# Kernel tuning notes

Measured on AMD Instinct MI355X. Metric: run time of the kernel, lower is better.

Reference implementation:

```python
import jax, jax.numpy as jnp
import numpy as np

EPS_OT = 0.1        # args.model.ot_reg
N_ITERS = 5         # args.model.ot_transport
COS_EPS = 1e-8      # torch F.cosine_similarity eps
L2_EPS = 1e-12      # torch F.normalize eps
LN_EPS = 1e-5       # nn.LayerNorm default eps
IN_DIM, HID = 768, 256


def setup_inputs() -> dict:
    key = jax.random.key(0)
    ks = jax.random.split(key, 8)
    Ba, Bb, Sa, Sb = 48, 48, 96, 96
    s_in = 1.0 / np.sqrt(IN_DIM)
    return {
        "batch_a": jax.random.normal(ks[0], (Ba, Sa, IN_DIM), jnp.float32),
        "batch_b": jax.random.normal(ks[1], (Bb, Sb, IN_DIM), jnp.float32),
        "Wq": jax.random.normal(ks[2], (IN_DIM, HID), jnp.float32) * s_in,
        "bq": jnp.zeros((HID,), jnp.float32),
        "Wk": jax.random.normal(ks[3], (IN_DIM, HID), jnp.float32) * s_in,
        "bk": jnp.zeros((HID,), jnp.float32),
        "Wv": jax.random.normal(ks[4], (IN_DIM, HID), jnp.float32) * s_in,
        "bv": jnp.zeros((HID,), jnp.float32),
        "ln_g": jnp.ones((HID,), jnp.float32),
        "ln_b": jnp.zeros((HID,), jnp.float32),
    }


def _layernorm(x, g, b):
    mu = jnp.mean(x, axis=-1, keepdims=True)
    var = jnp.var(x, axis=-1, keepdims=True)
    return (x - mu) * jax.lax.rsqrt(var + LN_EPS) * g + b


def _sinkhorn(C):
    # multiplicative Sinkhorn on kernel exp(C/eps); row/col renormalization
    T = jnp.exp(C / EPS_OT)  # [Ba,Bb,Sa,Sb]
    def body(_, T):
        T = T / jnp.sum(T, axis=-1, keepdims=True)
        T = T / jnp.sum(T, axis=-2, keepdims=True)
        return T
    return jax.lax.fori_loop(0, N_ITERS, body, T)


def reference(batch_a, batch_b, Wq, bq, Wk, bk, Wv, bv, ln_g, ln_b):
    q = batch_a @ Wq + bq          # [Ba,Sa,H]
    k = batch_b @ Wk + bk          # [Bb,Sb,H]
    v = batch_b @ Wv + bv          # [Bb,Sb,H]

    # cosine similarity across batches: [Ba,Bb,Sa,Sb]
    qn = q / jnp.maximum(jnp.linalg.norm(q, axis=-1, keepdims=True), COS_EPS)
    kn = k / jnp.maximum(jnp.linalg.norm(k, axis=-1, keepdims=True), COS_EPS)
    C = jnp.einsum('aid,bjd->abij', qn, kn)

    T = jax.lax.stop_gradient(_sinkhorn(C))  # C.detach() in source
    # F.normalize(dim=-1): L2 over last dim
    T = T / jnp.maximum(jnp.linalg.norm(T, axis=-1, keepdims=True), L2_EPS)
    # dropout p=0.0 -> identity (eval)

    attended = jnp.einsum('abij,bjd->abid', T, v) + q[:, None]  # [Ba,Bb,Sa,H]
    return _layernorm(attended, ln_g, ln_b)
```

## Files before the change

kernel.cpp:

```cpp
#include <hip/hip_runtime.h>
#include <hip/hip_bf16.h>

typedef __attribute__((ext_vector_type(4))) float f32x4;
typedef __attribute__((ext_vector_type(2))) float f32x2;
typedef __attribute__((ext_vector_type(8))) short bf16x8;
typedef __attribute__((ext_vector_type(4))) short s16x4;

#define BA 48
#define BB 48
#define SS 96
#define DIN 768
#define HH 256

static __device__ __forceinline__ short f2bf(float f) {
    __hip_bfloat16 h = __float2bfloat16(f);
    return *reinterpret_cast<short*>(&h);
}

static __device__ __forceinline__ f32x4 mfma16(bf16x8 a, bf16x8 b, f32x4 c) {
    return __builtin_amdgcn_mfma_f32_16x16x32_bf16(a, b, c, 0, 0, 0);
}

__global__ __launch_bounds__(256) void wt_kernel(
    const float* __restrict__ Wq, const float* __restrict__ Wk,
    const float* __restrict__ Wv, short* __restrict__ wt) {
    __shared__ float tile[64][65];
    int k0 = blockIdx.x * 64, n0 = blockIdx.y * 64, mat = blockIdx.z;
    const float* W = (mat == 0) ? Wq : (mat == 1) ? Wk : Wv;
    int t = threadIdx.x;
#pragma unroll
    for (int j = 0; j < 16; ++j) {
        int kk = j * 4 + (t >> 6);
        int nn = t & 63;
        tile[kk][nn] = W[(size_t)(k0 + kk) * HH + n0 + nn];
    }
    __syncthreads();
#pragma unroll
    for (int j = 0; j < 4; ++j) {
        int nn = j * 16 + (t >> 4);
        int kk = (t & 15) * 4;
        s16x4 pk;
#pragma unroll
        for (int i = 0; i < 4; ++i) pk[i] = f2bf(tile[kk + i][nn]);
        *reinterpret_cast<s16x4*>(&wt[(size_t)(mat * HH + n0 + nn) * DIN + k0 + kk]) = pk;
    }
}

__global__ __launch_bounds__(256) void xbf_kernel(
    const float* __restrict__ Xa, const float* __restrict__ Xb,
    short* __restrict__ xa, short* __restrict__ xb) {
    size_t i = (size_t)blockIdx.x * 256 + threadIdx.x;
    const float* src;
    short* dst;
    size_t off;
    if (i < 442368) { src = Xa; dst = xa; off = i * 8; }
    else            { src = Xb; dst = xb; off = (i - 442368) * 8; }
    f32x4 a = *reinterpret_cast<const f32x4*>(src + off);
    f32x4 b = *reinterpret_cast<const f32x4*>(src + off + 4);
    bf16x8 o;
    o[0] = f2bf(a[0]); o[1] = f2bf(a[1]); o[2] = f2bf(a[2]); o[3] = f2bf(a[3]);
    o[4] = f2bf(b[0]); o[5] = f2bf(b[1]); o[6] = f2bf(b[2]); o[7] = f2bf(b[3]);
    *reinterpret_cast<bf16x8*>(dst + off) = o;
}

__global__ __launch_bounds__(384) void qkv_kernel(
    const short* __restrict__ xa, const short* __restrict__ xb,
    const float* __restrict__ bq, const float* __restrict__ bk, const float* __restrict__ bv,
    const short* __restrict__ wt,
    float* __restrict__ q_ws, float* __restrict__ k_ws, short* __restrict__ vt_ws) {
    __shared__ short vtile[64][104];

    int bb = blockIdx.x;
    int mat = blockIdx.y;
    int c0 = blockIdx.z * 64;
    int tid = threadIdx.x;
    int wave = tid >> 6, lane = tid & 63;
    int c = lane & 15, g = lane >> 4;

    const short* X = ((mat == 0) ? xa : xb) + (size_t)bb * SS * DIN;
    const short* Wt = wt + (size_t)mat * HH * DIN;
    const float* bias = (mat == 0) ? bq : (mat == 1) ? bk : bv;

    const f32x4 z4 = {0.f, 0.f, 0.f, 0.f};
    f32x4 acc[4];
#pragma unroll
    for (int n = 0; n < 4; ++n) acc[n] = z4;

    const short* ap = X + (16 * wave + c) * DIN + g * 8;
    const short* bp = Wt + (c0 + c) * DIN + g * 8;
    for (int kk = 0; kk < DIN; kk += 32) {
        bf16x8 af = *reinterpret_cast<const bf16x8*>(ap + kk);
#pragma unroll
        for (int n = 0; n < 4; ++n) {
            bf16x8 bf = *reinterpret_cast<const bf16x8*>(bp + n * 16 * DIN + kk);
            acc[n] = mfma16(af, bf, acc[n]);
        }
    }
#pragma unroll
    for (int n = 0; n < 4; ++n) {
        float bv_ = bias[c0 + n * 16 + c];
#pragma unroll
        for (int r = 0; r < 4; ++r) acc[n][r] += bv_;
    }

    if (mat < 2) {
        float* dst = (mat == 0) ? q_ws : k_ws;
#pragma unroll
        for (int n = 0; n < 4; ++n)
#pragma unroll
            for (int r = 0; r < 4; ++r)
                dst[(bb * SS + 16 * wave + 4 * g + r) * HH + c0 + n * 16 + c] = acc[n][r];
    } else {
#pragma unroll
        for (int n = 0; n < 4; ++n)
#pragma unroll
            for (int r = 0; r < 4; ++r)
                vtile[n * 16 + c][16 * wave + 4 * g + r] = f2bf(acc[n][r]);
        __syncthreads();
#pragma unroll
        for (int t2 = 0; t2 < 2; ++t2) {
            int t = tid + t2 * 384;
            int d = t / 12, ch = t % 12;
            bf16x8 pk = *reinterpret_cast<const bf16x8*>(&vtile[d][ch * 8]);
            *reinterpret_cast<bf16x8*>(vt_ws + ((size_t)(bb * HH) + c0 + d) * SS + ch * 8) = pk;
        }
    }
}

__global__ __launch_bounds__(256) void norm_kernel(
    const float* __restrict__ q_ws, const float* __restrict__ k_ws,
    short* __restrict__ qn_ws, short* __restrict__ kn_ws) {
    int row = blockIdx.x * 4 + (threadIdx.x >> 6);
    int lane = threadIdx.x & 63;
    int isq = (row < 4608);
    const float* src = isq ? q_ws : k_ws;
    short* dst = isq ? qn_ws : kn_ws;
    int r = isq ? row : row - 4608;

    f32x4 v = *reinterpret_cast<const f32x4*>(src + (size_t)r * HH + lane * 4);
    float s = v[0] * v[0] + v[1] * v[1] + v[2] * v[2] + v[3] * v[3];
#pragma unroll
    for (int m = 1; m < 64; m <<= 1) s += __shfl_xor(s, m);
    float inv = 1.0f / fmaxf(sqrtf(s), 1e-8f);
    s16x4 o;
#pragma unroll
    for (int j = 0; j < 4; ++j) o[j] = f2bf(v[j] * inv);
    *reinterpret_cast<s16x4*>(dst + (size_t)r * HH + lane * 4) = o;
}

__global__ __launch_bounds__(256, 2) void sink_kernel(
    const short* __restrict__ qn_ws, const short* __restrict__ kn_ws,
    short* __restrict__ t_ws, int a_off) {
    int wave = threadIdx.x >> 6, lane = threadIdx.x & 63;
    int c = lane & 15, g = lane >> 4;
    int b = blockIdx.x * 4 + wave;
    int al = blockIdx.y;
    int a = al + a_off;

    const short* qbase = qn_ws + (size_t)(a * SS) * HH + c * HH + g * 8;
    const short* kbase = kn_ws + (size_t)(b * SS) * HH + c * HH + g * 8;

    const f32x4 z4 = {0.f, 0.f, 0.f, 0.f};
    f32x4 K[6][6];
#pragma unroll
    for (int ti = 0; ti < 6; ++ti)
#pragma unroll
        for (int tj = 0; tj < 6; ++tj) K[ti][tj] = z4;

#pragma unroll
    for (int kk = 0; kk < 8; ++kk) {
        bf16x8 qf[6];
#pragma unroll
        for (int ti = 0; ti < 6; ++ti)
            qf[ti] = *reinterpret_cast<const bf16x8*>(qbase + ti * 16 * HH + kk * 32);
#pragma unroll
        for (int tj = 0; tj < 6; ++tj) {
            bf16x8 kf = *reinterpret_cast<const bf16x8*>(kbase + tj * 16 * HH + kk * 32);
#pragma unroll
            for (int ti = 0; ti < 6; ++ti)
                K[ti][tj] = mfma16(kf, qf[ti], K[ti][tj]);
        }
    }

#pragma unroll
    for (int ti = 0; ti < 6; ++ti)
#pragma unroll
        for (int tj = 0; tj < 6; ++tj)
#pragma unroll
            for (int r = 0; r < 4; ++r)
                K[ti][tj][r] = exp2f(K[ti][tj][r] * 14.4269504088896341f);

#pragma unroll 1
    for (int it = 0; it < 5; ++it) {
#pragma unroll
        for (int ti = 0; ti < 6; ++ti) {
            float s0 = (K[ti][0][0] + K[ti][0][1]) + (K[ti][0][2] + K[ti][0][3]);
            float s1 = (K[ti][1][0] + K[ti][1][1]) + (K[ti][1][2] + K[ti][1][3]);
            float s2 = (K[ti][2][0] + K[ti][2][1]) + (K[ti][2][2] + K[ti][2][3]);
            float s3 = (K[ti][3][0] + K[ti][3][1]) + (K[ti][3][2] + K[ti][3][3]);
            float s4 = (K[ti][4][0] + K[ti][4][1]) + (K[ti][4][2] + K[ti][4][3]);
            float s5 = (K[ti][5][0] + K[ti][5][1]) + (K[ti][5][2] + K[ti][5][3]);
            float rs = ((s0 + s1) + (s2 + s3)) + (s4 + s5);
            rs += __shfl_xor(rs, 16);
            rs += __shfl_xor(rs, 32);
            float rinv = 1.0f / rs;
#pragma unroll
            for (int tj = 0; tj < 6; ++tj)
#pragma unroll
                for (int r = 0; r < 4; ++r) K[ti][tj][r] *= rinv;
        }
#pragma unroll
        for (int tj = 0; tj < 6; ++tj) {
            f32x4 cs;
#pragma unroll
            for (int r = 0; r < 4; ++r) {
                float u0 = K[0][tj][r] + K[1][tj][r];
                float u1 = K[2][tj][r] + K[3][tj][r];
                float u2 = K[4][tj][r] + K[5][tj][r];
                cs[r] = (u0 + u1) + u2;
            }
#pragma unroll
            for (int m = 1; m < 16; m <<= 1)
#pragma unroll
                for (int r = 0; r < 4; ++r) cs[r] += __shfl_xor(cs[r], m);
#pragma unroll
            for (int r = 0; r < 4; ++r) cs[r] = 1.0f / cs[r];
#pragma unroll
            for (int ti = 0; ti < 6; ++ti)
#pragma unroll
                for (int r = 0; r < 4; ++r) K[ti][tj][r] *= cs[r];
        }
    }

    short* tp = t_ws + (size_t)(al * BB + b) * SS * SS;
#pragma unroll
    for (int ti = 0; ti < 6; ++ti) {
        float s0 = 0.f, s1 = 0.f, s2 = 0.f;
#pragma unroll
        for (int tj = 0; tj < 2; ++tj)
#pragma unroll
            for (int r = 0; r < 4; ++r) s0 += K[ti][tj][r] * K[ti][tj][r];
#pragma unroll
        for (int tj = 2; tj < 4; ++tj)
#pragma unroll
            for (int r = 0; r < 4; ++r) s1 += K[ti][tj][r] * K[ti][tj][r];
#pragma unroll
        for (int tj = 4; tj < 6; ++tj)
#pragma unroll
            for (int r = 0; r < 4; ++r) s2 += K[ti][tj][r] * K[ti][tj][r];
        float ss = (s0 + s1) + s2;
        ss += __shfl_xor(ss, 16);
        ss += __shfl_xor(ss, 32);
        float linv = 1.0f / fmaxf(sqrtf(ss), 1e-12f);
#pragma unroll
        for (int tj = 0; tj < 6; ++tj) {
            s16x4 pk;
#pragma unroll
            for (int r = 0; r < 4; ++r) pk[r] = f2bf(K[ti][tj][r] * linv);
            *reinterpret_cast<s16x4*>(tp + (16 * ti + c) * SS + 16 * tj + 4 * g) = pk;
        }
    }
}

__global__ __launch_bounds__(768, 6) void pv_kernel(
    const short* __restrict__ t_ws, const short* __restrict__ vt_ws,
    const float* __restrict__ q_ws,
    const float* __restrict__ ln_g, const float* __restrict__ ln_b,
    float* __restrict__ out, int a_off) {
    __shared__ float stats[2][2][SS];
    __shared__ float etile[12][4][136];

    int b = blockIdx.x, al = blockIdx.y;
    int a = al + a_off;
    int tid = threadIdx.x;
    int wave = tid >> 6, lane = tid & 63;
    int rt = wave % 6, h = wave / 6;
    int c = lane & 15, g = lane >> 4;

    const f32x4 z4 = {0.f, 0.f, 0.f, 0.f};
    f32x4 acc[8];
#pragma unroll
    for (int n = 0; n < 8; ++n) acc[n] = z4;

    const short* tp = t_ws + ((size_t)(al * BB + b)) * SS * SS + (16 * rt + c) * SS + g * 8;
    const short* vp = vt_ws + ((size_t)(b * HH) + 128 * h + c) * SS + g * 8;
#pragma unroll
    for (int ks = 0; ks < 3; ++ks) {
        bf16x8 af = *reinterpret_cast<const bf16x8*>(tp + ks * 32);
#pragma unroll
        for (int n = 0; n < 8; ++n) {
            bf16x8 bf = *reinterpret_cast<const bf16x8*>(vp + n * 16 * SS + ks * 32);
            acc[n] = mfma16(af, bf, acc[n]);
        }
    }

    const float* qa = q_ws + (size_t)a * SS * HH + 128 * h;
    int r0 = 16 * rt + 4 * g;
    float s1[4] = {0.f, 0.f, 0.f, 0.f};
    float s2[4] = {0.f, 0.f, 0.f, 0.f};
#pragma unroll
    for (int n = 0; n < 8; ++n)
#pragma unroll
        for (int r = 0; r < 4; ++r) {
            float x = acc[n][r] + qa[(r0 + r) * HH + n * 16 + c];
            acc[n][r] = x;
            s1[r] += x;
            s2[r] += x * x;
        }
#pragma unroll
    for (int m = 1; m < 16; m <<= 1)
#pragma unroll
        for (int r = 0; r < 4; ++r) {
            s1[r] += __shfl_xor(s1[r], m);
            s2[r] += __shfl_xor(s2[r], m);
        }
    if (c == 0) {
#pragma unroll
        for (int r = 0; r < 4; ++r) {
            stats[h][0][r0 + r] = s1[r];
            stats[h][1][r0 + r] = s2[r];
        }
    }
    __syncthreads();
    float mean[4], inv[4];
#pragma unroll
    for (int r = 0; r < 4; ++r) {
        float t1 = stats[0][0][r0 + r] + stats[1][0][r0 + r];
        float t2 = stats[0][1][r0 + r] + stats[1][1][r0 + r];
        mean[r] = t1 * (1.0f / 256.0f);
        float var = t2 * (1.0f / 256.0f) - mean[r] * mean[r];
        inv[r] = rsqrtf(var + 1e-5f);
    }

    f32x2 g2 = *reinterpret_cast<const f32x2*>(ln_g + 128 * h + 2 * lane);
    f32x2 b2 = *reinterpret_cast<const f32x2*>(ln_b + 128 * h + 2 * lane);
    float* ob = out + ((size_t)(a * BB + b)) * SS * HH + 128 * h;
#pragma unroll
    for (int r = 0; r < 4; ++r) {
#pragma unroll
        for (int n = 0; n < 8; ++n)
            etile[wave][g][n * 16 + c] = (acc[n][r] - mean[r]) * inv[r];
#pragma unroll
        for (int t = 0; t < 4; ++t) {
            f32x2 x2 = *reinterpret_cast<const f32x2*>(&etile[wave][t][2 * lane]);
            *reinterpret_cast<f32x2*>(ob + (size_t)(16 * rt + 4 * t + r) * HH + 2 * lane) =
                x2 * g2 + b2;
        }
    }
}

extern "C" void kernel_launch(void* const* d_in, const int* in_sizes, int n_in,
                              void* d_out, int out_size, void* d_ws, size_t ws_size,
                              hipStream_t stream) {
    const float* Xa = (const float*)d_in[0];
    const float* Xb = (const float*)d_in[1];
    const float* Wq = (const float*)d_in[2];
    const float* bq = (const float*)d_in[3];
    const float* Wk = (const float*)d_in[4];
    const float* bk = (const float*)d_in[5];
    const float* Wv = (const float*)d_in[6];
    const float* bv = (const float*)d_in[7];
    const float* ln_g = (const float*)d_in[8];
    const float* ln_b = (const float*)d_in[9];
    float* out = (float*)d_out;

    char* ws = (char*)d_ws;
    short* wt    = (short*)(ws);
    short* xa_bf = (short*)(ws + 1179648);
    short* xb_bf = (short*)(ws + 8257536);
    float* q_ws  = (float*)(ws + 15335424);
    float* k_ws  = (float*)(ws + 20054016);
    short* qn_ws = (short*)(ws + 24772608);
    short* kn_ws = (short*)(ws + 27131904);
    short* vt_ws = (short*)(ws + 29491200);

    const size_t t_full = (size_t)BA * BB * SS * SS * 2;
    size_t t_off = 31850496;
    size_t avail = (ws_size > t_off) ? ws_size - t_off : 0;
    int nch;
    if (avail >= t_full) nch = 1;
    else if (avail >= t_full / 2) nch = 2;
    else if (avail >= t_full / 4) nch = 4;
    else { nch = 4; t_off = 0; }
    short* t_ws = (short*)(ws + t_off);
    int apc = BA / nch;

    wt_kernel<<<dim3(12, 4, 3), dim3(256), 0, stream>>>(Wq, Wk, Wv, wt);
    xbf_kernel<<<dim3(3456), dim3(256), 0, stream>>>(Xa, Xb, xa_bf, xb_bf);
    qkv_kernel<<<dim3(BA, 3, 4), dim3(384), 0, stream>>>(xa_bf, xb_bf, bq, bk, bv, wt,
                                                         q_ws, k_ws, vt_ws);
    norm_kernel<<<dim3(2304), dim3(256), 0, stream>>>(q_ws, k_ws, qn_ws, kn_ws);
    for (int ch = 0; ch < nch; ++ch) {
        sink_kernel<<<dim3(12, apc), dim3(256), 0, stream>>>(qn_ws, kn_ws, t_ws, ch * apc);
        pv_kernel<<<dim3(BB, apc), dim3(768), 0, stream>>>(t_ws, vt_ws, q_ws,
                                                           ln_g, ln_b, out, ch * apc);
    }
}
```

Before: 247.4 us.

## Use scaling-vector Sinkhorn and halve QKV column tile for more blocks

The Sinkhorn loop no longer rescales the full 96x96 register tile every half-iteration. It keeps row scalings u and column scalings v and computes row and column sums as K·v and Kᵀ·u, applying them only once at the final L2 normalization. This cuts per-iteration multiply work roughly in half but adds multiplies inside each sum. Separately, the QKV projection now uses 32-column tiles instead of 64, doubling the grid to raise occupancy, at the cost of more A-operand reloads.

```diff
diff --git a/kernel.cpp b/kernel.cpp
--- a/kernel.cpp
+++ b/kernel.cpp
@@ -68,11 +68,11 @@
     const float* __restrict__ bq, const float* __restrict__ bk, const float* __restrict__ bv,
     const short* __restrict__ wt,
     float* __restrict__ q_ws, float* __restrict__ k_ws, short* __restrict__ vt_ws) {
-    __shared__ short vtile[64][104];
+    __shared__ short vtile[32][104];
 
     int bb = blockIdx.x;
     int mat = blockIdx.y;
-    int c0 = blockIdx.z * 64;
+    int c0 = blockIdx.z * 32;
     int tid = threadIdx.x;
     int wave = tid >> 6, lane = tid & 63;
     int c = lane & 15, g = lane >> 4;
@@ -82,22 +82,21 @@
     const float* bias = (mat == 0) ? bq : (mat == 1) ? bk : bv;
 
     const f32x4 z4 = {0.f, 0.f, 0.f, 0.f};
-    f32x4 acc[4];
-#pragma unroll
-    for (int n = 0; n < 4; ++n) acc[n] = z4;
+    f32x4 acc[2];
+    acc[0] = z4; acc[1] = z4;
 
     const short* ap = X + (16 * wave + c) * DIN + g * 8;
     const short* bp = Wt + (c0 + c) * DIN + g * 8;
     for (int kk = 0; kk < DIN; kk += 32) {
         bf16x8 af = *reinterpret_cast<const bf16x8*>(ap + kk);
 #pragma unroll
-        for (int n = 0; n < 4; ++n) {
+        for (int n = 0; n < 2; ++n) {
             bf16x8 bf = *reinterpret_cast<const bf16x8*>(bp + n * 16 * DIN + kk);
             acc[n] = mfma16(af, bf, acc[n]);
         }
     }
 #pragma unroll
-    for (int n = 0; n < 4; ++n) {
+    for (int n = 0; n < 2; ++n) {
         float bv_ = bias[c0 + n * 16 + c];
 #pragma unroll
         for (int r = 0; r < 4; ++r) acc[n][r] += bv_;
@@ -106,20 +105,19 @@
     if (mat < 2) {
         float* dst = (mat == 0) ? q_ws : k_ws;
 #pragma unroll
-        for (int n = 0; n < 4; ++n)
+        for (int n = 0; n < 2; ++n)
 #pragma unroll
             for (int r = 0; r < 4; ++r)
                 dst[(bb * SS + 16 * wave + 4 * g + r) * HH + c0 + n * 16 + c] = acc[n][r];
     } else {
 #pragma unroll
-        for (int n = 0; n < 4; ++n)
+        for (int n = 0; n < 2; ++n)
 #pragma unroll
             for (int r = 0; r < 4; ++r)
                 vtile[n * 16 + c][16 * wave + 4 * g + r] = f2bf(acc[n][r]);
         __syncthreads();
-#pragma unroll
-        for (int t2 = 0; t2 < 2; ++t2) {
-            int t = tid + t2 * 384;
+        {
+            int t = tid;
             int d = t / 12, ch = t % 12;
             bf16x8 pk = *reinterpret_cast<const bf16x8*>(&vtile[d][ch * 8]);
             *reinterpret_cast<bf16x8*>(vt_ws + ((size_t)(bb * HH) + c0 + d) * SS + ch * 8) = pk;
@@ -190,65 +188,50 @@
             for (int r = 0; r < 4; ++r)
                 K[ti][tj][r] = exp2f(K[ti][tj][r] * 14.4269504088896341f);
 
+    f32x4 v[6];
+#pragma unroll
+    for (int tj = 0; tj < 6; ++tj) v[tj] = (f32x4){1.f, 1.f, 1.f, 1.f};
+    float u[6];
+
 #pragma unroll 1
     for (int it = 0; it < 5; ++it) {
 #pragma unroll
         for (int ti = 0; ti < 6; ++ti) {
-            float s0 = (K[ti][0][0] + K[ti][0][1]) + (K[ti][0][2] + K[ti][0][3]);
-            float s1 = (K[ti][1][0] + K[ti][1][1]) + (K[ti][1][2] + K[ti][1][3]);
-            float s2 = (K[ti][2][0] + K[ti][2][1]) + (K[ti][2][2] + K[ti][2][3]);
-            float s3 = (K[ti][3][0] + K[ti][3][1]) + (K[ti][3][2] + K[ti][3][3]);
-            float s4 = (K[ti][4][0] + K[ti][4][1]) + (K[ti][4][2] + K[ti][4][3]);
-            float s5 = (K[ti][5][0] + K[ti][5][1]) + (K[ti][5][2] + K[ti][5][3]);
-            float rs = ((s0 + s1) + (s2 + s3)) + (s4 + s5);
+            f32x4 p0 = K[ti][0] * v[0] + K[ti][1] * v[1];
+            f32x4 p1 = K[ti][2] * v[2] + K[ti][3] * v[3];
+            f32x4 p2 = K[ti][4] * v[4] + K[ti][5] * v[5];
+            f32x4 p = (p0 + p1) + p2;
+            float rs = (p[0] + p[1]) + (p[2] + p[3]);
             rs += __shfl_xor(rs, 16);
             rs += __shfl_xor(rs, 32);
-            float rinv = 1.0f / rs;
-#pragma unroll
-            for (int tj = 0; tj < 6; ++tj)
-#pragma unroll
-                for (int r = 0; r < 4; ++r) K[ti][tj][r] *= rinv;
+            u[ti] = 1.0f / rs;
         }
 #pragma unroll
         for (int tj = 0; tj < 6; ++tj) {
-            f32x4 cs;
-#pragma unroll
-            for (int r = 0; r < 4; ++r) {
-                float u0 = K[0][tj][r] + K[1][tj][r];
-                float u1 = K[2][tj][r] + K[3][tj][r];
-                float u2 = K[4][tj][r] + K[5][tj][r];
-                cs[r] = (u0 + u1) + u2;
-            }
+            f32x4 c0 = K[0][tj] * u[0] + K[1][tj] * u[1];
+            f32x4 c1 = K[2][tj] * u[2] + K[3][tj] * u[3];
+            f32x4 c2 = K[4][tj] * u[4] + K[5][tj] * u[5];
+            f32x4 cs = (c0 + c1) + c2;
 #pragma unroll
             for (int m = 1; m < 16; m <<= 1)
 #pragma unroll
                 for (int r = 0; r < 4; ++r) cs[r] += __shfl_xor(cs[r], m);
 #pragma unroll
-            for (int r = 0; r < 4; ++r) cs[r] = 1.0f / cs[r];
-#pragma unroll
-            for (int ti = 0; ti < 6; ++ti)
-#pragma unroll
-                for (int r = 0; r < 4; ++r) K[ti][tj][r] *= cs[r];
+            for (int r = 0; r < 4; ++r) v[tj][r] = 1.0f / cs[r];
         }
     }
 
     short* tp = t_ws + (size_t)(al * BB + b) * SS * SS;
 #pragma unroll
     for (int ti = 0; ti < 6; ++ti) {
-        float s0 = 0.f, s1 = 0.f, s2 = 0.f;
-#pragma unroll
-        for (int tj = 0; tj < 2; ++tj)
-#pragma unroll
-            for (int r = 0; r < 4; ++r) s0 += K[ti][tj][r] * K[ti][tj][r];
-#pragma unroll
-        for (int tj = 2; tj < 4; ++tj)
-#pragma unroll
-            for (int r = 0; r < 4; ++r) s1 += K[ti][tj][r] * K[ti][tj][r];
-#pragma unroll
-        for (int tj = 4; tj < 6; ++tj)
-#pragma unroll
-            for (int r = 0; r < 4; ++r) s2 += K[ti][tj][r] * K[ti][tj][r];
-        float ss = (s0 + s1) + s2;
+        f32x4 w[6];
+#pragma unroll
+        for (int tj = 0; tj < 6; ++tj) w[tj] = K[ti][tj] * v[tj];
+        f32x4 q0 = w[0] * w[0] + w[1] * w[1];
+        f32x4 q1 = w[2] * w[2] + w[3] * w[3];
+        f32x4 q2 = w[4] * w[4] + w[5] * w[5];
+        f32x4 qq = (q0 + q1) + q2;
+        float ss = (qq[0] + qq[1]) + (qq[2] + qq[3]);
         ss += __shfl_xor(ss, 16);
         ss += __shfl_xor(ss, 32);
         float linv = 1.0f / fmaxf(sqrtf(ss), 1e-12f);
@@ -256,7 +239,7 @@
         for (int tj = 0; tj < 6; ++tj) {
             s16x4 pk;
 #pragma unroll
-            for (int r = 0; r < 4; ++r) pk[r] = f2bf(K[ti][tj][r] * linv);
+            for (int r = 0; r < 4; ++r) pk[r] = f2bf(w[tj][r] * linv);
             *reinterpret_cast<s16x4*>(tp + (16 * ti + c) * SS + 16 * tj + 4 * g) = pk;
         }
     }
@@ -387,7 +370,7 @@
 
     wt_kernel<<<dim3(12, 4, 3), dim3(256), 0, stream>>>(Wq, Wk, Wv, wt);
     xbf_kernel<<<dim3(3456), dim3(256), 0, stream>>>(Xa, Xb, xa_bf, xb_bf);
-    qkv_kernel<<<dim3(BA, 3, 4), dim3(384), 0, stream>>>(xa_bf, xb_bf, bq, bk, bv, wt,
+    qkv_kernel<<<dim3(BA, 3, 8), dim3(384), 0, stream>>>(xa_bf, xb_bf, bq, bk, bv, wt,
                                                          q_ws, k_ws, vt_ws);
     norm_kernel<<<dim3(2304), dim3(256), 0, stream>>>(q_ws, k_ws, qn_ws, kn_ws);
     for (int ch = 0; ch < nch; ++ch) {
```

After: 241.9 us. 1.02x faster.
